# Optimization experiments

Hardware: AMD Instinct MI355X
Metric: run time of the kernel (lower is better)

## Reference

```python
import jax, jax.numpy as jnp
import numpy as np

jax.config.update("jax_enable_x64", True)  # original casts to double for cov/cholesky

B, C, H, W, DR = 64, 2048, 14, 14, 256
EPS = 1e-6      # LCMCOV eps added to covariance diagonal
BN_EPS = 1e-5   # torch BatchNorm2d default eps


def setup_inputs() -> dict:
    key = jax.random.key(0)
    k0, k1 = jax.random.split(key)
    x = jax.random.normal(k0, (B, C, H, W), dtype=jnp.float32)
    # 1x1 conv weight (kaiming fan_out for relu): std = sqrt(2 / fan_out), fan_out = DR*1*1... torch uses fan_out = out_ch*k*k per output; approximate with sqrt(2/C) scale on (DR, C)
    w_conv = jax.random.normal(k1, (DR, C), dtype=jnp.float32) * np.sqrt(2.0 / C).astype(np.float32)
    gamma = jnp.ones((DR,), jnp.float32)
    beta = jnp.zeros((DR,), jnp.float32)
    run_mean = jnp.zeros((DR,), jnp.float32)
    run_var = jnp.ones((DR,), jnp.float32)
    return {"x": x, "w_conv": w_conv, "gamma": gamma, "beta": beta,
            "run_mean": run_mean, "run_var": run_var}


def reference(x, w_conv, gamma, beta, run_mean, run_var):
    b, c, h, w = x.shape
    dr = w_conv.shape[0]
    m = h * w
    # 1x1 conv (no bias) + BatchNorm2d (eval mode, running stats) + ReLU
    y = jnp.einsum('bchw,dc->bdhw', x, w_conv)
    scale = gamma / jnp.sqrt(run_var + BN_EPS)
    y = y * scale[None, :, None, None] + (beta - run_mean * scale)[None, :, None, None]
    y = jax.nn.relu(y)
    # Covpool in float64: x I_hat x^T == (1/M) * (x - mean)(x - mean)^T
    xd = y.reshape(b, dr, m).astype(jnp.float64)
    xc = xd - xd.mean(axis=2, keepdims=True)  # [B, DR, M]
    cov = jnp.einsum('bdm,bem->bde', xc, xc) / m  # [B, DR, DR]
    # LogI_LCM: Cholesky, log the diagonal, symmetrize
    cov = cov + EPS * jnp.eye(dr, dtype=jnp.float64)
    L = jnp.linalg.cholesky(cov)
    diag = jnp.log(jnp.diagonal(L, axis1=-2, axis2=-1))          # [B, DR]
    tril = jnp.tril(L, -1) + jnp.eye(dr, dtype=L.dtype) * diag[:, :, None]
    sym = tril + jnp.swapaxes(tril, -1, -2)
    # Triuvec: upper-triangular (incl diag) entries in row-major order, cast to float32
    iu, ju = jnp.triu_indices(dr)
    return sym[:, iu, ju].astype(jnp.float32)  # [B, DR*(DR+1)/2]
```

## Files before the change

### kernel.cpp

```cpp
#include <hip/hip_runtime.h>
#include <math.h>

#define BB 64
#define CC 2048
#define MM 196
#define DD 256
#define NTOT (BB * MM)

__global__ __launch_bounds__(256) void k_conv(
    const float* __restrict__ x, const float* __restrict__ w,
    const float* __restrict__ gamma, const float* __restrict__ beta,
    const float* __restrict__ rmean, const float* __restrict__ rvar,
    float* __restrict__ yt) {
  const int tid = threadIdx.x;
  const int tx = tid & 15;
  const int ty = tid >> 4;
  const int n0 = blockIdx.x * 64;
  const int d0 = blockIdx.y * 64;

  __shared__ float Ws[32][66];
  __shared__ float Xs[32][64];

  float acc[4][4];
#pragma unroll
  for (int i = 0; i < 4; ++i)
#pragma unroll
    for (int j = 0; j < 4; ++j) acc[i][j] = 0.f;

  const int cW = tid & 31;
  const int dW = tid >> 5;
  const int nX = tid & 63;
  const int kX = tid >> 6;
  const int gn = n0 + nX;
  const int bX = gn / MM;
  const int mX = gn - bX * MM;
  const float* xptr = x + (size_t)bX * CC * MM + mX;

  float wreg[8], xreg[8];
#pragma unroll
  for (int p = 0; p < 8; ++p)
    wreg[p] = w[(size_t)(d0 + dW + p * 8) * CC + cW];
#pragma unroll
  for (int p = 0; p < 8; ++p)
    xreg[p] = xptr[(size_t)(kX + p * 4) * MM];

  for (int k0 = 0; k0 < CC; k0 += 32) {
    __syncthreads();
#pragma unroll
    for (int p = 0; p < 8; ++p) Ws[cW][dW + p * 8] = wreg[p];
#pragma unroll
    for (int p = 0; p < 8; ++p) Xs[kX + p * 4][nX] = xreg[p];
    __syncthreads();
    if (k0 + 32 < CC) {
#pragma unroll
      for (int p = 0; p < 8; ++p)
        wreg[p] = w[(size_t)(d0 + dW + p * 8) * CC + (k0 + 32) + cW];
#pragma unroll
      for (int p = 0; p < 8; ++p)
        xreg[p] = xptr[(size_t)(k0 + 32 + kX + p * 4) * MM];
    }
#pragma unroll
    for (int k = 0; k < 32; ++k) {
      float a[4], bv[4];
#pragma unroll
      for (int i = 0; i < 4; ++i) a[i] = Ws[k][ty * 4 + i];
#pragma unroll
      for (int j = 0; j < 4; ++j) bv[j] = Xs[k][tx * 4 + j];
#pragma unroll
      for (int i = 0; i < 4; ++i)
#pragma unroll
        for (int j = 0; j < 4; ++j) acc[i][j] = fmaf(a[i], bv[j], acc[i][j]);
    }
  }

  float scl[4], sft[4];
#pragma unroll
  for (int i = 0; i < 4; ++i) {
    int d = d0 + ty * 4 + i;
    float s = gamma[d] / sqrtf(rvar[d] + 1e-5f);
    scl[i] = s;
    sft[i] = beta[d] - rmean[d] * s;
  }
#pragma unroll
  for (int j = 0; j < 4; ++j) {
    int n = n0 + tx * 4 + j;
    int b = n / MM;
    int m = n - b * MM;
    float* yrow = yt + ((size_t)b * MM + m) * DD + d0 + ty * 4;
#pragma unroll
    for (int i = 0; i < 4; ++i) {
      float v = fmaf(acc[i][j], scl[i], sft[i]);
      yrow[i] = v > 0.f ? v : 0.f;
    }
  }
}

__global__ __launch_bounds__(256) void k_means(const float* __restrict__ yt,
                                               double* __restrict__ mean) {
  const int b = blockIdx.x;
  const int d = threadIdx.x;
  const float* p = yt + (size_t)b * MM * DD + d;
  double s0 = 0, s1 = 0, s2 = 0, s3 = 0;
  for (int m = 0; m < MM; m += 4) {
    s0 += (double)p[(size_t)(m + 0) * DD];
    s1 += (double)p[(size_t)(m + 1) * DD];
    s2 += (double)p[(size_t)(m + 2) * DD];
    s3 += (double)p[(size_t)(m + 3) * DD];
  }
  mean[b * DD + d] = (s0 + s1 + s2 + s3) * (1.0 / MM);
}

__global__ __launch_bounds__(256) void k_cov(const float* __restrict__ yt,
                                             const double* __restrict__ mean,
                                             double* __restrict__ cov) {
  const int b = blockIdx.x;
  const int t = blockIdx.y;
  const int ti = (t < 1) ? 0 : (t < 3) ? 1 : (t < 6) ? 2 : 3;
  const int tj = t - (ti * (ti + 1)) / 2;
  const int i0 = ti * 64, j0 = tj * 64;
  const int tid = threadIdx.x;
  const int tx = tid & 15, ty = tid >> 4;

  __shared__ double As[32][66];
  __shared__ double Bs[32][66];

  double acc[4][4];
#pragma unroll
  for (int i = 0; i < 4; ++i)
#pragma unroll
    for (int j = 0; j < 4; ++j) acc[i][j] = 0.0;

  const int dl = tid & 63, kl = tid >> 6;
  const double mA = mean[b * DD + i0 + dl];
  const double mB = mean[b * DD + j0 + dl];
  const float* ybase = yt + (size_t)b * MM * DD;

  for (int k0 = 0; k0 < MM; k0 += 32) {
    __syncthreads();
#pragma unroll
    for (int p = 0; p < 8; ++p) {
      int k = kl + p * 4;
      int m = k0 + k;
      double av = 0.0, bv = 0.0;
      if (m < MM) {
        av = (double)ybase[(size_t)m * DD + i0 + dl] - mA;
        bv = (double)ybase[(size_t)m * DD + j0 + dl] - mB;
      }
      As[k][dl] = av;
      Bs[k][dl] = bv;
    }
    __syncthreads();
#pragma unroll
    for (int k = 0; k < 32; ++k) {
      double a[4], bv[4];
#pragma unroll
      for (int i = 0; i < 4; ++i) a[i] = As[k][ty * 4 + i];
#pragma unroll
      for (int j = 0; j < 4; ++j) bv[j] = Bs[k][tx * 4 + j];
#pragma unroll
      for (int i = 0; i < 4; ++i)
#pragma unroll
        for (int j = 0; j < 4; ++j) acc[i][j] = fma(a[i], bv[j], acc[i][j]);
    }
  }

  double* cb = cov + (size_t)b * DD * DD;
#pragma unroll
  for (int i = 0; i < 4; ++i) {
#pragma unroll
    for (int j = 0; j < 4; ++j) {
      int gi = i0 + ty * 4 + i, gj = j0 + tx * 4 + j;
      double v = acc[i][j] * (1.0 / MM);
      if (gi == gj) v += 1e-6;
      cb[(size_t)gi * DD + gj] = v;
      if (ti != tj) cb[(size_t)gj * DD + gi] = v;
    }
  }
}

__global__ __launch_bounds__(256) void k_panel2(double* __restrict__ cov,
                                                int kb) {
  const int b = blockIdx.x;
  double* A = cov + (size_t)b * DD * DD;
  const int j0 = kb * 32;
  const int tid = threadIdx.x;

  __shared__ double Sp[256][33];
  __shared__ double Lp[224][33];
  __shared__ double L11s[32][33];
  __shared__ double rpivs[32];

  if (blockIdx.y == 0) {
    const int R = DD - j0;
    const int pj = j0 - 32;

    for (int e = tid; e < R * 32; e += 256) {
      int r = e >> 5, c = e & 31;
      Sp[r][c] = A[(size_t)(j0 + r) * DD + j0 + c];
      if (kb > 0) Lp[r][c] = A[(size_t)(j0 + r) * DD + pj + c];
    }
    __syncthreads();

    if (kb > 0) {
      const int cg = tid & 7;
      const int rg = tid >> 3;
      const int c0 = cg * 4;
      for (int r = rg; r < R; r += 32) {
        double a0 = 0, a1 = 0, a2 = 0, a3 = 0;
#pragma unroll
        for (int p = 0; p < 32; ++p) {
          double lr = Lp[r][p];
          a0 = fma(lr, Lp[c0 + 0][p], a0);
          a1 = fma(lr, Lp[c0 + 1][p], a1);
          a2 = fma(lr, Lp[c0 + 2][p], a2);
          a3 = fma(lr, Lp[c0 + 3][p], a3);
        }
        Sp[r][c0 + 0] -= a0;
        Sp[r][c0 + 1] -= a1;
        Sp[r][c0 + 2] -= a2;
        Sp[r][c0 + 3] -= a3;
      }
    }
    __syncthreads();

    if (tid < 32) {
      double r[32];
#pragma unroll
      for (int k = 0; k < 32; ++k) r[k] = Sp[tid][k];
      double rpkeep = 0.0;
#pragma unroll
      for (int j = 0; j < 32; ++j) {
        double dj = __shfl(r[j], j);
        double piv = sqrt(dj);
        double rp = 1.0 / piv;
        if (tid == j) {
          r[j] = piv;
          rpkeep = rp;
        } else {
          r[j] = r[j] * rp;
        }
        double lij = r[j];
#pragma unroll
        for (int k = j + 1; k < 32; ++k) {
          double ck = __shfl(lij, k);
          r[k] -= lij * ck;
        }
      }
#pragma unroll
      for (int k = 0; k < 32; ++k) L11s[tid][k] = (k <= tid) ? r[k] : 0.0;
      rpivs[tid] = rpkeep;
      for (int k = 0; k <= tid; ++k)
        A[(size_t)(j0 + tid) * DD + j0 + k] = r[k];
    }
    __syncthreads();

    const int T = R - 32;
    if (tid < T) {
      double q[32];
#pragma unroll
      for (int k = 0; k < 32; ++k) q[k] = Sp[32 + tid][k];
#pragma unroll
      for (int j = 0; j < 32; ++j) {
        double s = q[j];
#pragma unroll
        for (int k = 0; k < 32; ++k)
          if (k < j) s -= q[k] * L11s[j][k];
        q[j] = s * rpivs[j];
      }
      double* dst = &A[(size_t)(j0 + 32 + tid) * DD + j0];
#pragma unroll
      for (int k = 0; k < 32; ++k) dst[k] = q[k];
    }
  } else {
    const int o = j0 + 32;
    const int S = DD - o;
    const int pj = j0 - 32;
    int tI = 0, tJ = (int)blockIdx.y - 1;
    while (tJ > tI) {
      tJ -= (tI + 1);
      tI++;
    }
    const int i0 = tI * 64, jj0 = tJ * 64;
    const int tx = tid & 15, ty = tid >> 4;

    double(*Ea)[33] = (double(*)[33])(&Lp[0][0]);
    double(*Eb)[33] = (double(*)[33])(&Lp[64][0]);

    for (int e = tid; e < 64 * 32; e += 256) {
      int r = e >> 5, c = e & 31;
      Ea[r][c] =
          (i0 + r < S) ? A[(size_t)(o + i0 + r) * DD + pj + c] : 0.0;
      Eb[r][c] =
          (jj0 + r < S) ? A[(size_t)(o + jj0 + r) * DD + pj + c] : 0.0;
    }
    __syncthreads();

    double s[4][4];
#pragma unroll
    for (int i = 0; i < 4; ++i)
#pragma unroll
      for (int j = 0; j < 4; ++j) s[i][j] = 0.0;

    const int bi = ty * 4, bj = tx * 4;
#pragma unroll
    for (int k = 0; k < 32; ++k) {
      double a[4], bv[4];
#pragma unroll
      for (int i = 0; i < 4; ++i) a[i] = Ea[bi + i][k];
#pragma unroll
      for (int j = 0; j < 4; ++j) bv[j] = Eb[bj + j][k];
#pragma unroll
      for (int i = 0; i < 4; ++i)
#pragma unroll
        for (int j = 0; j < 4; ++j) s[i][j] = fma(a[i], bv[j], s[i][j]);
    }

#pragma unroll
    for (int i = 0; i < 4; ++i)
#pragma unroll
      for (int j = 0; j < 4; ++j) {
        int gi = i0 + bi + i, gj = jj0 + bj + j;
        if (gi < S && gj < S && gi >= gj)
          A[(size_t)(o + gi) * DD + (o + gj)] -= s[i][j];
      }
  }
}

__global__ __launch_bounds__(256) void k_out(const double* __restrict__ cov,
                                             float* __restrict__ out) {
  const int b = blockIdx.y;
  int t = blockIdx.x;
  int ti = 0, tj = t;
  while (tj >= 4 - ti) {
    tj -= (4 - ti);
    ti++;
  }
  tj += ti;
  const int tid = threadIdx.x;
  const double* A = cov + (size_t)b * DD * DD;

  __shared__ float S[64][65];
  for (int e = tid; e < 4096; e += 256) {
    int jj = e >> 6, ii = e & 63;
    S[jj][ii] = (float)A[(size_t)(tj * 64 + jj) * DD + ti * 64 + ii];
  }
  __syncthreads();

  for (int e = tid; e < 4096; e += 256) {
    int ii = e >> 6, jj = e & 63;
    int i = ti * 64 + ii, j = tj * 64 + jj;
    if (j < i) continue;
    float v = S[jj][ii];
    if (i == j) v = 2.0f * logf(v);
    int off = i * DD - (i * (i - 1)) / 2 + (j - i);
    out[(size_t)b * 32896 + off] = v;
  }
}

extern "C" void kernel_launch(void* const* d_in, const int* in_sizes, int n_in,
                              void* d_out, int out_size, void* d_ws,
                              size_t ws_size, hipStream_t stream) {
  const float* x = (const float*)d_in[0];
  const float* w = (const float*)d_in[1];
  const float* gamma = (const float*)d_in[2];
  const float* beta = (const float*)d_in[3];
  const float* rmean = (const float*)d_in[4];
  const float* rvar = (const float*)d_in[5];
  float* out = (float*)d_out;

  char* ws = (char*)d_ws;
  float* yt = (float*)ws;
  double* mean = (double*)(ws + 12845056);
  double* cov = (double*)(ws + 12845056 + 131072);

  k_conv<<<dim3(NTOT / 64, DD / 64), 256, 0, stream>>>(x, w, gamma, beta,
                                                       rmean, rvar, yt);
  k_means<<<BB, 256, 0, stream>>>(yt, mean);
  k_cov<<<dim3(BB, 10), 256, 0, stream>>>(yt, mean, cov);
  for (int kb = 0; kb < 8; ++kb) {
    int ntiles = 0;
    if (kb > 0) {
      int S = DD - (kb * 32 + 32);
      if (S > 0) {
        int nt = (S + 63) / 64;
        ntiles = nt * (nt + 1) / 2;
      }
    }
    k_panel2<<<dim3(BB, 1 + ntiles), 256, 0, stream>>>(cov, kb);
  }
  k_out<<<dim3(10, BB), 256, 0, stream>>>(cov, out);
}
```

Measured before the change: 720.4 us.

## Use split-bf16 MFMA for the 1x1 conv GEMM with a weight prep kernel

Moves the fp32 FMA-based 1x1 convolution GEMM onto bf16 MFMA instructions. Both the weights and the activations are split into high and low bf16 parts, and three MFMAs per tile approximate fp32 precision. A new prep kernel converts the weights once per call and precomputes the BN scale and shift. Each block now covers all 256 output channels for 64 positions, loading A fragments directly from global memory. The cost is extra conversion work, a small precision loss compared with true fp32, and reuse of the cov workspace for the split weights, which is safe only because the prep and conv kernels run before cov is written.

```diff
diff --git a/kernel.cpp b/kernel.cpp
--- a/kernel.cpp
+++ b/kernel.cpp
@@ -7,90 +7,160 @@
 #define DD 256
 #define NTOT (BB * MM)
 
-__global__ __launch_bounds__(256) void k_conv(
-    const float* __restrict__ x, const float* __restrict__ w,
-    const float* __restrict__ gamma, const float* __restrict__ beta,
-    const float* __restrict__ rmean, const float* __restrict__ rvar,
-    float* __restrict__ yt) {
+typedef __attribute__((ext_vector_type(8))) short short8;
+typedef __attribute__((ext_vector_type(4))) short short4v;
+typedef __attribute__((ext_vector_type(4))) unsigned short ushort4v;
+typedef __attribute__((ext_vector_type(4))) float f32x4;
+
+__device__ __forceinline__ unsigned short bf16_rne(float f) {
+  unsigned int u = __float_as_uint(f);
+  unsigned int r = u + 0x7FFFu + ((u >> 16) & 1u);
+  return (unsigned short)(r >> 16);
+}
+
+__global__ __launch_bounds__(256) void k_prep(
+    const float* __restrict__ w, const float* __restrict__ gamma,
+    const float* __restrict__ beta, const float* __restrict__ rmean,
+    const float* __restrict__ rvar, unsigned short* __restrict__ wh,
+    unsigned short* __restrict__ wl, float* __restrict__ sclv,
+    float* __restrict__ sftv) {
+  const int e0 = (blockIdx.x * 256 + threadIdx.x) * 4;
+  f32x4 v = *(const f32x4*)(w + e0);
+  ushort4v h, l;
+#pragma unroll
+  for (int i = 0; i < 4; ++i) {
+    unsigned short hb = bf16_rne(v[i]);
+    float hf = __uint_as_float((unsigned int)hb << 16);
+    h[i] = hb;
+    l[i] = bf16_rne(v[i] - hf);
+  }
+  *(ushort4v*)(wh + e0) = h;
+  *(ushort4v*)(wl + e0) = l;
+  if (blockIdx.x == 0 && threadIdx.x < DD) {
+    int d = threadIdx.x;
+    float s = gamma[d] / sqrtf(rvar[d] + 1e-5f);
+    sclv[d] = s;
+    sftv[d] = beta[d] - rmean[d] * s;
+  }
+}
+
+__global__ __launch_bounds__(256, 2) void k_conv(
+    const float* __restrict__ x, const unsigned short* __restrict__ wh,
+    const unsigned short* __restrict__ wl, const float* __restrict__ sclv,
+    const float* __restrict__ sftv, float* __restrict__ yt) {
   const int tid = threadIdx.x;
-  const int tx = tid & 15;
-  const int ty = tid >> 4;
+  const int wid = tid >> 6, lane = tid & 63;
+  const int quad = lane >> 4, l16 = lane & 15;
   const int n0 = blockIdx.x * 64;
-  const int d0 = blockIdx.y * 64;
-
-  __shared__ float Ws[32][66];
-  __shared__ float Xs[32][64];
-
-  float acc[4][4];
+
+  __shared__ unsigned short Xh[64][36];
+  __shared__ unsigned short Xl[64][36];
+
+  f32x4 acc[4][4];
 #pragma unroll
   for (int i = 0; i < 4; ++i)
 #pragma unroll
-    for (int j = 0; j < 4; ++j) acc[i][j] = 0.f;
-
-  const int cW = tid & 31;
-  const int dW = tid >> 5;
-  const int nX = tid & 63;
-  const int kX = tid >> 6;
+    for (int j = 0; j < 4; ++j) acc[i][j] = (f32x4)0.f;
+
+  const int nX = tid & 63, kq = tid >> 6;
   const int gn = n0 + nX;
-  const int bX = gn / MM;
-  const int mX = gn - bX * MM;
-  const float* xptr = x + (size_t)bX * CC * MM + mX;
-
-  float wreg[8], xreg[8];
-#pragma unroll
-  for (int p = 0; p < 8; ++p)
-    wreg[p] = w[(size_t)(d0 + dW + p * 8) * CC + cW];
-#pragma unroll
-  for (int p = 0; p < 8; ++p)
-    xreg[p] = xptr[(size_t)(kX + p * 4) * MM];
-
-  for (int k0 = 0; k0 < CC; k0 += 32) {
-    __syncthreads();
-#pragma unroll
-    for (int p = 0; p < 8; ++p) Ws[cW][dW + p * 8] = wreg[p];
-#pragma unroll
-    for (int p = 0; p < 8; ++p) Xs[kX + p * 4][nX] = xreg[p];
-    __syncthreads();
-    if (k0 + 32 < CC) {
+  const int bX = gn / MM, mX = gn - bX * MM;
+  const float* xp = x + (size_t)bX * CC * MM + mX;
+
+  float xr[8];
+#pragma unroll
+  for (int p = 0; p < 8; ++p) xr[p] = xp[(size_t)(kq * 8 + p) * MM];
+
+  size_t aoff[4];
+#pragma unroll
+  for (int ds = 0; ds < 4; ++ds)
+    aoff[ds] = (size_t)(wid * 64 + ds * 16 + l16) * CC + quad * 8;
+
+  short8 Ah[4], Al[4], Ah2[4], Al2[4];
+#pragma unroll
+  for (int ds = 0; ds < 4; ++ds) {
+    Ah[ds] = *(const short8*)(wh + aoff[ds]);
+    Al[ds] = *(const short8*)(wl + aoff[ds]);
+  }
+
+  for (int c = 0; c < 64; ++c) {
+    const int k0 = c * 32;
+    __syncthreads();
+    {
+      ushort4v h0, h1, l0, l1;
+#pragma unroll
+      for (int p = 0; p < 4; ++p) {
+        unsigned short hb = bf16_rne(xr[p]);
+        float hf = __uint_as_float((unsigned int)hb << 16);
+        h0[p] = hb;
+        l0[p] = bf16_rne(xr[p] - hf);
+      }
+#pragma unroll
+      for (int p = 0; p < 4; ++p) {
+        unsigned short hb = bf16_rne(xr[4 + p]);
+        float hf = __uint_as_float((unsigned int)hb << 16);
+        h1[p] = hb;
+        l1[p] = bf16_rne(xr[4 + p] - hf);
+      }
+      *(ushort4v*)&Xh[nX][kq * 8] = h0;
+      *(ushort4v*)&Xh[nX][kq * 8 + 4] = h1;
+      *(ushort4v*)&Xl[nX][kq * 8] = l0;
+      *(ushort4v*)&Xl[nX][kq * 8 + 4] = l1;
+    }
+    __syncthreads();
+    if (c < 63) {
 #pragma unroll
       for (int p = 0; p < 8; ++p)
-        wreg[p] = w[(size_t)(d0 + dW + p * 8) * CC + (k0 + 32) + cW];
-#pragma unroll
-      for (int p = 0; p < 8; ++p)
-        xreg[p] = xptr[(size_t)(k0 + 32 + kX + p * 4) * MM];
-    }
-#pragma unroll
-    for (int k = 0; k < 32; ++k) {
-      float a[4], bv[4];
-#pragma unroll
-      for (int i = 0; i < 4; ++i) a[i] = Ws[k][ty * 4 + i];
-#pragma unroll
-      for (int j = 0; j < 4; ++j) bv[j] = Xs[k][tx * 4 + j];
-#pragma unroll
-      for (int i = 0; i < 4; ++i)
-#pragma unroll
-        for (int j = 0; j < 4; ++j) acc[i][j] = fmaf(a[i], bv[j], acc[i][j]);
-    }
-  }
-
-  float scl[4], sft[4];
-#pragma unroll
-  for (int i = 0; i < 4; ++i) {
-    int d = d0 + ty * 4 + i;
-    float s = gamma[d] / sqrtf(rvar[d] + 1e-5f);
-    scl[i] = s;
-    sft[i] = beta[d] - rmean[d] * s;
-  }
-#pragma unroll
-  for (int j = 0; j < 4; ++j) {
-    int n = n0 + tx * 4 + j;
-    int b = n / MM;
-    int m = n - b * MM;
-    float* yrow = yt + ((size_t)b * MM + m) * DD + d0 + ty * 4;
-#pragma unroll
-    for (int i = 0; i < 4; ++i) {
-      float v = fmaf(acc[i][j], scl[i], sft[i]);
-      yrow[i] = v > 0.f ? v : 0.f;
+        xr[p] = xp[(size_t)(k0 + 32 + kq * 8 + p) * MM];
+#pragma unroll
+      for (int ds = 0; ds < 4; ++ds) {
+        Ah2[ds] = *(const short8*)(wh + aoff[ds] + k0 + 32);
+        Al2[ds] = *(const short8*)(wl + aoff[ds] + k0 + 32);
+      }
+    }
+#pragma unroll
+    for (int ns = 0; ns < 4; ++ns) {
+      const unsigned short* bp = &Xh[ns * 16 + l16][quad * 8];
+      short4v b0 = *(const short4v*)bp;
+      short4v b1 = *(const short4v*)(bp + 4);
+      short8 Bh = __builtin_shufflevector(b0, b1, 0, 1, 2, 3, 4, 5, 6, 7);
+      const unsigned short* bq = &Xl[ns * 16 + l16][quad * 8];
+      short4v c0 = *(const short4v*)bq;
+      short4v c1 = *(const short4v*)(bq + 4);
+      short8 Bl = __builtin_shufflevector(c0, c1, 0, 1, 2, 3, 4, 5, 6, 7);
+#pragma unroll
+      for (int ds = 0; ds < 4; ++ds) {
+        acc[ds][ns] = __builtin_amdgcn_mfma_f32_16x16x32_bf16(
+            Ah[ds], Bh, acc[ds][ns], 0, 0, 0);
+        acc[ds][ns] = __builtin_amdgcn_mfma_f32_16x16x32_bf16(
+            Ah[ds], Bl, acc[ds][ns], 0, 0, 0);
+        acc[ds][ns] = __builtin_amdgcn_mfma_f32_16x16x32_bf16(
+            Al[ds], Bh, acc[ds][ns], 0, 0, 0);
+      }
+    }
+#pragma unroll
+    for (int ds = 0; ds < 4; ++ds) {
+      Ah[ds] = Ah2[ds];
+      Al[ds] = Al2[ds];
+    }
+  }
+
+#pragma unroll
+  for (int ds = 0; ds < 4; ++ds) {
+    const int dbase = wid * 64 + ds * 16 + quad * 4;
+    f32x4 s4 = *(const f32x4*)(sclv + dbase);
+    f32x4 f4 = *(const f32x4*)(sftv + dbase);
+#pragma unroll
+    for (int ns = 0; ns < 4; ++ns) {
+      const int n = n0 + ns * 16 + l16;
+      const int b = n / MM, m = n - b * MM;
+      f32x4 o;
+#pragma unroll
+      for (int r = 0; r < 4; ++r) {
+        float v = fmaf(acc[ds][ns][r], s4[r], f4[r]);
+        o[r] = v > 0.f ? v : 0.f;
+      }
+      *(f32x4*)(yt + ((size_t)b * MM + m) * DD + dbase) = o;
     }
   }
 }
@@ -281,17 +351,15 @@
       tI++;
     }
     const int i0 = tI * 64, jj0 = tJ * 64;
-    const int tx = tid & 15, ty = tid >> 4;
+    const int txl = tid & 15, tyl = tid >> 4;
 
     double(*Ea)[33] = (double(*)[33])(&Lp[0][0]);
     double(*Eb)[33] = (double(*)[33])(&Lp[64][0]);
 
     for (int e = tid; e < 64 * 32; e += 256) {
       int r = e >> 5, c = e & 31;
-      Ea[r][c] =
-          (i0 + r < S) ? A[(size_t)(o + i0 + r) * DD + pj + c] : 0.0;
-      Eb[r][c] =
-          (jj0 + r < S) ? A[(size_t)(o + jj0 + r) * DD + pj + c] : 0.0;
+      Ea[r][c] = (i0 + r < S) ? A[(size_t)(o + i0 + r) * DD + pj + c] : 0.0;
+      Eb[r][c] = (jj0 + r < S) ? A[(size_t)(o + jj0 + r) * DD + pj + c] : 0.0;
     }
     __syncthreads();
 
@@ -301,7 +369,7 @@
 #pragma unroll
       for (int j = 0; j < 4; ++j) s[i][j] = 0.0;
 
-    const int bi = ty * 4, bj = tx * 4;
+    const int bi = tyl * 4, bj = txl * 4;
 #pragma unroll
     for (int k = 0; k < 32; ++k) {
       double a[4], bv[4];
@@ -372,9 +440,14 @@
   float* yt = (float*)ws;
   double* mean = (double*)(ws + 12845056);
   double* cov = (double*)(ws + 12845056 + 131072);
-
-  k_conv<<<dim3(NTOT / 64, DD / 64), 256, 0, stream>>>(x, w, gamma, beta,
-                                                       rmean, rvar, yt);
+  unsigned short* wh = (unsigned short*)cov;
+  unsigned short* wl = wh + (DD * CC);
+  float* sclv = (float*)(wl + (DD * CC));
+  float* sftv = sclv + DD;
+
+  k_prep<<<512, 256, 0, stream>>>(w, gamma, beta, rmean, rvar, wh, wl, sclv,
+                                  sftv);
+  k_conv<<<NTOT / 64, 256, 0, stream>>>(x, wh, wl, sclv, sftv, yt);
   k_means<<<BB, 256, 0, stream>>>(yt, mean);
   k_cov<<<dim3(BB, 10), 256, 0, stream>>>(yt, mean, cov);
   for (int kb = 0; kb < 8; ++kb) {
```

New measurement: 627.9 us. -12.8%, faster.
